# Kernel tuning notes

Measured on AMD Instinct MI355X. Metric: run time of the kernel, lower is better.

## Reference

```python
import jax, jax.numpy as jnp
import numpy as np

N_QUBITS = 4
NOISE_RATE = 0.01  # depolarizing channel scales Pauli-Z expectation by (1 - p)


def _rx_mat(theta):
    # RX(theta) = [[cos(t/2), -i sin(t/2)], [-i sin(t/2), cos(t/2)]]; theta scalar or (b,)
    c = jnp.cos(theta / 2).astype(jnp.complex64)
    s = (-1j * jnp.sin(theta / 2)).astype(jnp.complex64)
    return jnp.stack([jnp.stack([c, s], -1), jnp.stack([s, c], -1)], -2)


def _apply_1q(state, mat, wire):
    # state: (b, 2,2,2,2); mat: (2,2) shared or (b,2,2) per-sample
    st = jnp.moveaxis(state, wire + 1, -1)
    if mat.ndim == 2:
        st = st @ mat.T
    else:
        st = jnp.einsum('b...j,bij->b...i', st, mat)
    return jnp.moveaxis(st, -1, wire + 1)


def _cnot(state, src, tgt):
    st = jnp.moveaxis(state, (src + 1, tgt + 1), (-2, -1))
    st = jnp.concatenate([st[..., 0:1, :], st[..., 1:2, ::-1]], axis=-2)
    return jnp.moveaxis(st, (-2, -1), (src + 1, tgt + 1))


def _qlayer(x, theta):
    # x: (b, n_qubits) encoding angles; theta: (n_params,) trainable RX angles
    b = x.shape[0]
    state = jnp.zeros((b,) + (2,) * N_QUBITS, jnp.complex64)
    state = state.at[(slice(None),) + (0,) * N_QUBITS].set(1.0)
    for w in range(N_QUBITS):                      # GeneralEncoder: RX(x_w) on wire w
        state = _apply_1q(state, _rx_mat(x[:, w]), w)
    for k in range(theta.shape[0]):                # trainable RX_k on wire k
        state = _apply_1q(state, _rx_mat(theta[k]), k)
    for i in range(N_QUBITS):                      # CNOT ring (i, (i+1)%n)
        state = _cnot(state, i, (i + 1) % N_QUBITS)
    p = jnp.abs(state) ** 2                        # (b, 2,2,2,2)
    ez = []
    for w in range(N_QUBITS):                      # <Z_w> = P(0) - P(1)
        axes = tuple(a for a in range(1, N_QUBITS + 1) if a != w + 1)
        m = p.sum(axes)
        ez.append(m[:, 0] - m[:, 1])
    return (1.0 - NOISE_RATE) * jnp.stack(ez, -1)  # depolarizing noise on expectations


def reference(inputs, w_lin, b_lin, w_map, b_map, theta):
    # inputs: (S, B, D); gate order: forget, input, update, output
    S, B, D = inputs.shape
    H = w_map.shape[1]
    hx0 = jnp.zeros((B, H), inputs.dtype)
    cx0 = jnp.zeros((B, H), inputs.dtype)
    qbatch = jax.vmap(_qlayer)  # over the 4 gates

    def step(carry, x):
        hx, cx = carry
        comb = jnp.concatenate([x, hx], axis=1)                      # (B, D+H)
        pre = jnp.einsum('gqd,bd->gbq', w_lin, comb) + b_lin[:, None, :]
        q = qbatch(pre, theta)                                       # (4, B, n_qubits)
        acts = jnp.stack([jax.nn.sigmoid(q[0]), jax.nn.sigmoid(q[1]),
                          jnp.tanh(q[2]), jax.nn.sigmoid(q[3])])
        gates = jnp.einsum('ghq,gbq->gbh', w_map, acts) + b_map[:, None, :]
        f, i_, g, o = gates
        cx2 = f * cx + i_ * g
        hx2 = o * jnp.tanh(cx2)
        return (hx2, cx2), hx2

    (hx, cx), outputs = jax.lax.scan(step, (hx0, cx0), inputs)
    return outputs, hx, cx


def setup_inputs() -> dict:
    key = jax.random.key(0)
    ks = jax.random.split(key, 6)
    S, B, D, H, NQ, NG = 512, 256, 128, 256, 4, 4
    return {
        'inputs': jax.random.normal(ks[0], (S, B, D), jnp.float32),
        'w_lin': jax.random.normal(ks[1], (NG, NQ, D + H), jnp.float32) * 0.05,
        'b_lin': jax.random.normal(ks[2], (NG, NQ), jnp.float32) * 0.05,
        'w_map': jax.random.normal(ks[3], (NG, H, NQ), jnp.float32) * 0.3,
        'b_map': jax.random.normal(ks[4], (NG, H), jnp.float32) * 0.05,
        'theta': jax.random.uniform(ks[5], (NG, 4), jnp.float32, 0.0, 2.0 * np.pi),
    }
```

## Files before the change

### kernel.cpp

```cpp
#include <hip/hip_runtime.h>

#define SEQ   512
#define BATCH 256
#define DIN   128
#define XPAD  132
#define HID   256
#define NOISE 0.99f

__device__ __forceinline__ float dot4(float4 a, float4 b) {
    return fmaf(a.x, b.x, fmaf(a.y, b.y, fmaf(a.z, b.z, a.w * b.w)));
}
__device__ __forceinline__ float sigmoid_(float x) {
    return __builtin_amdgcn_rcpf(1.0f + __expf(-x));
}
__device__ __forceinline__ float tanh_(float x) {
    float ax = fabsf(x);
    float e  = __expf(2.0f * ax);
    float t  = __builtin_amdgcn_rcpf(e + 1.0f);
    float r  = 1.0f - 2.0f * t;
    return copysignf(r, x);
}
template <int CTRL>
__device__ __forceinline__ float dppmov(float v) {
    return __int_as_float(__builtin_amdgcn_mov_dpp(__float_as_int(v), CTRL, 0xF, 0xF, false));
}
__device__ __forceinline__ float swap16_sum(float v) {
    float a = v, b;
    asm("v_mov_b32 %1, %0\n\tv_permlane16_swap_b32 %0, %1" : "+v"(a), "=&v"(b));
    return a + b;
}
__device__ __forceinline__ float swap32_sum(float v) {
    float a = v, b;
    asm("v_mov_b32 %1, %0\n\tv_permlane32_swap_b32 %0, %1" : "+v"(a), "=&v"(b));
    return a + b;
}
__device__ __forceinline__ void barrier_lds() {
    asm volatile("s_waitcnt lgkmcnt(0)\n\ts_barrier" ::: "memory");
}

__global__ __launch_bounds__(256, 1) void qlstm_fused(
    const float* __restrict__ x,
    const float* __restrict__ w_lin,
    const float* __restrict__ b_lin,
    const float* __restrict__ w_map,
    const float* __restrict__ b_map,
    const float* __restrict__ theta,
    float* __restrict__ out)
{
    const int b = blockIdx.x;
    const int t = threadIdx.x;

    __shared__ __align__(16) float pre_lds[SEQ * 16];
    __shared__ __align__(16) float wlds[16 * 132];
    __shared__ __align__(16) float x_chunk[2][16][XPAD];
    __shared__ __align__(16) float hx_lds[HID];
    __shared__ __align__(16) float acts_lds[16];

    for (int i = t; i < 16 * 128; i += 256) {
        int pp = i >> 7, dd = i & 127;
        wlds[pp * 132 + dd] = w_lin[pp * 384 + dd];
    }

    const int xr_ = t >> 5;
    const int xc_ = (t & 31) << 2;
    auto xld = [&](int c, int r) -> float4 {
        return *(const float4*)(x + ((size_t)((c << 4) + r) * BATCH + b) * DIN + xc_);
    };

    float4 ra = xld(0, xr_), rb = xld(0, xr_ + 8);
    *(float4*)&x_chunk[0][xr_][xc_]     = ra;
    *(float4*)&x_chunk[0][xr_ + 8][xc_] = rb;
    ra = xld(1, xr_); rb = xld(1, xr_ + 8);
    barrier_lds();

    const int sp = t >> 4;
    const int pp = t & 15;
    const float* wr = &wlds[pp * 132];
    const float bt = b_lin[pp] + theta[pp];

    for (int c = 0; c < 32; ++c) {
        const float* xrow = x_chunk[c & 1][sp];
        float acc = bt;
        #pragma unroll 8
        for (int d = 0; d < 32; ++d)
            acc += dot4(*(const float4*)(xrow + d * 4), *(const float4*)(wr + d * 4));
        pre_lds[((c << 4) + sp) * 16 + pp] = acc;

        if (c + 1 < 32) {
            *(float4*)&x_chunk[(c + 1) & 1][xr_][xc_]     = ra;
            *(float4*)&x_chunk[(c + 1) & 1][xr_ + 8][xc_] = rb;
            if (c + 2 < 32) { ra = xld(c + 2, xr_); rb = xld(c + 2, xr_ + 8); }
        }
        barrier_lds();
    }

    const int l = t & 63;
    const int g = t >> 6;
    const int q = l & 3;
    const int j = l >> 2;
    const int p = (g << 2) | q;

    const int sig = (j >> 1) & 3;
    const float* wp = w_lin + p * 384 + 128 + j * 16;
    const float4 wh0 = *(const float4*)(wp + ((0 ^ sig) << 2));
    const float4 wh1 = *(const float4*)(wp + ((1 ^ sig) << 2));
    const float4 wh2 = *(const float4*)(wp + ((2 ^ sig) << 2));
    const float4 wh3 = *(const float4*)(wp + ((3 ^ sig) << 2));

    const float4 wm0 = ((const float4*)w_map)[0 * 256 + t];
    const float4 wm1 = ((const float4*)w_map)[1 * 256 + t];
    const float4 wm2 = ((const float4*)w_map)[2 * 256 + t];
    const float4 wm3 = ((const float4*)w_map)[3 * 256 + t];
    const float bm0 = b_map[t];
    const float bm1 = b_map[256 + t];
    const float bm2 = b_map[512 + t];
    const float bm3 = b_map[768 + t];

    const float* hr = &hx_lds[j * 16];
    const float* hr0 = hr + ((0 ^ sig) << 2);
    const float* hr1 = hr + ((1 ^ sig) << 2);
    const float* hr2 = hr + ((2 ^ sig) << 2);
    const float* hr3 = hr + ((3 ^ sig) << 2);

    hx_lds[t] = 0.0f;
    float hx = 0.0f, cx = 0.0f;
    float* out_seq = out;
    float* out_hx  = out + (size_t)SEQ * BATCH * HID;
    float* out_cx  = out_hx + BATCH * HID;
    barrier_lds();

    float px0 = pre_lds[p];

    for (int s = 0; s < SEQ; ++s) {
        const float pxu = px0;
        const int s1 = (s + 1 < SEQ) ? s + 1 : SEQ - 1;
        px0 = pre_lds[s1 * 16 + p];

        const float4 ha0 = *(const float4*)hr0;
        const float4 ha1 = *(const float4*)hr1;
        const float4 ha2 = *(const float4*)hr2;
        const float4 ha3 = *(const float4*)hr3;
        float acc = dot4(wh0, ha0) + dot4(wh1, ha1)
                  + dot4(wh2, ha2) + dot4(wh3, ha3);
        acc += dppmov<0x124>(acc);
        acc += dppmov<0x128>(acc);
        acc  = swap16_sum(acc);
        acc  = swap32_sum(acc);

        const float A  = __cosf(acc + pxu);
        const float Bv = dppmov<0xB1>(A);
        const float Cv = dppmov<0x4E>(A);
        const float Dv = dppmov<0x4E>(Bv);

        const float t1 = Cv * Dv;
        const float u  = (q & 1) ? (A * Bv) : ((q == 2) ? A : Bv);
        const float v  = (q == 1) ? 1.0f : t1;
        const float ez = NOISE * u * v;
        const float act = (g == 2) ? tanh_(ez) : sigmoid_(ez);
        if (l < 4) acts_lds[(g << 2) | l] = act;
        barrier_lds();

        const float4 a0 = *(const float4*)&acts_lds[0];
        const float4 a1 = *(const float4*)&acts_lds[4];
        const float4 a2 = *(const float4*)&acts_lds[8];
        const float4 a3 = *(const float4*)&acts_lds[12];

        const float fv = bm0 + dot4(wm0, a0);
        const float iv = bm1 + dot4(wm1, a1);
        const float gv = bm2 + dot4(wm2, a2);
        const float ov = bm3 + dot4(wm3, a3);

        cx = fmaf(fv, cx, iv * gv);
        hx = ov * tanh_(cx);

        hx_lds[t] = hx;
        out_seq[((size_t)s * BATCH + b) * HID + t] = hx;
        barrier_lds();
    }

    out_hx[(size_t)b * HID + t] = hx;
    out_cx[(size_t)b * HID + t] = cx;
}

extern "C" void kernel_launch(void* const* d_in, const int* in_sizes, int n_in,
                              void* d_out, int out_size, void* d_ws, size_t ws_size,
                              hipStream_t stream) {
    const float* x     = (const float*)d_in[0];
    const float* w_lin = (const float*)d_in[1];
    const float* b_lin = (const float*)d_in[2];
    const float* w_map = (const float*)d_in[3];
    const float* b_map = (const float*)d_in[4];
    const float* theta = (const float*)d_in[5];
    float* out = (float*)d_out;

    qlstm_fused<<<dim3(BATCH), dim3(256), 0, stream>>>(
        x, w_lin, b_lin, w_map, b_map, theta, out);
}
```

Baseline: 251.0 us.

## Interleave input projection chunks into the recurrent loop instead of prologue

Only the first two chunks of the input projection are computed up front. The remaining 30 chunks are computed incrementally inside the sequential recurrence, two float4 dot products per step, with the x-chunk double buffer refilled every 16 steps. The aim is to hide the roughly 30-chunk prologue behind the latency-bound recurrent steps. In exchange, every step does extra LDS reads and work, and correctness depends on each chunk's pre_lds values being written before they are read. The hx_lds initialisation moves earlier and one barrier is dropped.

```diff
diff --git a/kernel.cpp b/kernel.cpp
--- a/kernel.cpp
+++ b/kernel.cpp
@@ -57,8 +57,8 @@
     __shared__ __align__(16) float acts_lds[16];
 
     for (int i = t; i < 16 * 128; i += 256) {
-        int pp = i >> 7, dd = i & 127;
-        wlds[pp * 132 + dd] = w_lin[pp * 384 + dd];
+        int pp_ = i >> 7, dd = i & 127;
+        wlds[pp_ * 132 + dd] = w_lin[pp_ * 384 + dd];
     }
 
     const int xr_ = t >> 5;
@@ -67,6 +67,8 @@
         return *(const float4*)(x + ((size_t)((c << 4) + r) * BATCH + b) * DIN + xc_);
     };
 
+    hx_lds[t] = 0.0f;
+
     float4 ra = xld(0, xr_), rb = xld(0, xr_ + 8);
     *(float4*)&x_chunk[0][xr_][xc_]     = ra;
     *(float4*)&x_chunk[0][xr_ + 8][xc_] = rb;
@@ -78,19 +80,17 @@
     const float* wr = &wlds[pp * 132];
     const float bt = b_lin[pp] + theta[pp];
 
-    for (int c = 0; c < 32; ++c) {
-        const float* xrow = x_chunk[c & 1][sp];
+    for (int c = 0; c < 2; ++c) {
+        const float* xrow = x_chunk[c][sp];
         float acc = bt;
         #pragma unroll 8
         for (int d = 0; d < 32; ++d)
             acc += dot4(*(const float4*)(xrow + d * 4), *(const float4*)(wr + d * 4));
         pre_lds[((c << 4) + sp) * 16 + pp] = acc;
 
-        if (c + 1 < 32) {
-            *(float4*)&x_chunk[(c + 1) & 1][xr_][xc_]     = ra;
-            *(float4*)&x_chunk[(c + 1) & 1][xr_ + 8][xc_] = rb;
-            if (c + 2 < 32) { ra = xld(c + 2, xr_); rb = xld(c + 2, xr_ + 8); }
-        }
+        *(float4*)&x_chunk[(c + 1) & 1][xr_][xc_]     = ra;
+        *(float4*)&x_chunk[(c + 1) & 1][xr_ + 8][xc_] = rb;
+        ra = xld(c + 2, xr_); rb = xld(c + 2, xr_ + 8);
         barrier_lds();
     }
 
@@ -122,12 +122,11 @@
     const float* hr2 = hr + ((2 ^ sig) << 2);
     const float* hr3 = hr + ((3 ^ sig) << 2);
 
-    hx_lds[t] = 0.0f;
     float hx = 0.0f, cx = 0.0f;
+    float pacc = bt;
     float* out_seq = out;
     float* out_hx  = out + (size_t)SEQ * BATCH * HID;
     float* out_cx  = out_hx + BATCH * HID;
-    barrier_lds();
 
     float px0 = pre_lds[p];
 
@@ -140,6 +139,28 @@
         const float4 ha1 = *(const float4*)hr1;
         const float4 ha2 = *(const float4*)hr2;
         const float4 ha3 = *(const float4*)hr3;
+
+        if (s < 480) {
+            const int k  = s & 15;
+            const int cc = (s >> 4) + 2;
+            if (k == 0) {
+                if (cc + 1 < 32) {
+                    *(float4*)&x_chunk[(cc + 1) & 1][xr_][xc_]     = ra;
+                    *(float4*)&x_chunk[(cc + 1) & 1][xr_ + 8][xc_] = rb;
+                }
+                if (cc + 2 < 32) {
+                    ra = xld(cc + 2, xr_); rb = xld(cc + 2, xr_ + 8);
+                }
+            }
+            const float* xrow = x_chunk[cc & 1][sp];
+            pacc += dot4(*(const float4*)(xrow + 8 * k),     *(const float4*)(wr + 8 * k));
+            pacc += dot4(*(const float4*)(xrow + 8 * k + 4), *(const float4*)(wr + 8 * k + 4));
+            if (k == 15) {
+                pre_lds[((cc << 4) + sp) * 16 + pp] = pacc;
+                pacc = bt;
+            }
+        }
+
         float acc = dot4(wh0, ha0) + dot4(wh1, ha1)
                   + dot4(wh2, ha2) + dot4(wh3, ha3);
         acc += dppmov<0x124>(acc);
```

Result: slower. 274.8 us (+9.5%).
